# Kernel optimization log

Measured on AMD Instinct MI355X. Metric: run time of the kernel, lower is better.

Reference implementation:

```python
import jax, jax.numpy as jnp
import numpy as np

ALPHA = 0.25
GAMMA = 2.0
W_CLASS, W_BBOX, W_GIOU, W_EMBED = 1.0, 1.0, 1.0, 0.5
EPS = 1e-8


def box_cxcywh_to_xyxy(b):
    cx, cy, w, h = b[..., 0], b[..., 1], b[..., 2], b[..., 3]
    return jnp.stack([cx - 0.5 * w, cy - 0.5 * h, cx + 0.5 * w, cy + 0.5 * h], axis=-1)


def generalized_box_iou(boxes1, boxes2):
    # boxes1 [N,4], boxes2 [M,4] in xyxy -> [N,M]
    area1 = (boxes1[:, 2] - boxes1[:, 0]) * (boxes1[:, 3] - boxes1[:, 1])
    area2 = (boxes2[:, 2] - boxes2[:, 0]) * (boxes2[:, 3] - boxes2[:, 1])
    lt = jnp.maximum(boxes1[:, None, :2], boxes2[None, :, :2])  # [N,M,2]
    rb = jnp.minimum(boxes1[:, None, 2:], boxes2[None, :, 2:])
    wh = jnp.clip(rb - lt, 0.0)
    inter = wh[..., 0] * wh[..., 1]
    union = area1[:, None] + area2[None, :] - inter
    iou = inter / union
    lt_e = jnp.minimum(boxes1[:, None, :2], boxes2[None, :, :2])
    rb_e = jnp.maximum(boxes1[:, None, 2:], boxes2[None, :, 2:])
    wh_e = jnp.clip(rb_e - lt_e, 0.0)
    area_e = wh_e[..., 0] * wh_e[..., 1]
    return iou - (area_e - union) / area_e


def setup_inputs() -> dict:
    key = jax.random.key(0)
    ks = jax.random.split(key, 6)
    B, Q, C, D, M = 16, 1024, 91, 512, 1600
    pred_logits = jax.random.normal(ks[0], (B, Q, C), dtype=jnp.float32)
    pred_boxes = jax.random.uniform(ks[1], (B, Q, 4), dtype=jnp.float32)
    pred_embed = jax.random.normal(ks[2], (B, Q, D), dtype=jnp.float32)
    text_embeddings = jax.random.normal(ks[3], (C, D), dtype=jnp.float32)
    tgt_ids = jax.random.randint(ks[4], (M,), 0, C, dtype=jnp.int64 if jax.config.jax_enable_x64 else jnp.int32)
    tgt_bbox = jax.random.uniform(ks[5], (M, 4), dtype=jnp.float32)
    return {
        'pred_logits': pred_logits,
        'pred_boxes': pred_boxes,
        'pred_embed': pred_embed,
        'text_embeddings': text_embeddings,
        'tgt_ids': tgt_ids,
        'tgt_bbox': tgt_bbox,
    }


def reference(pred_logits, pred_boxes, pred_embed, text_embeddings, tgt_ids, tgt_bbox):
    B, Q, _ = pred_logits.shape
    N = B * Q
    # --- focal class cost on gathered target-class columns: [N, M]
    logits = pred_logits.reshape(N, -1)
    p = jax.nn.sigmoid(logits[:, tgt_ids])
    pos_cost = ALPHA * (1.0 - p) ** GAMMA * (-jnp.log(p + EPS))
    neg_cost = (1.0 - ALPHA) * p ** GAMMA * (-jnp.log(1.0 - p + EPS))
    cost_class = pos_cost - neg_cost
    # --- L1 box cost (cdist, p=1): [N, M]
    out_bbox = pred_boxes.reshape(N, 4)
    cost_bbox = jnp.sum(jnp.abs(out_bbox[:, None, :] - tgt_bbox[None, :, :]), axis=-1)
    # --- GIoU cost: [N, M]
    cost_giou = -generalized_box_iou(box_cxcywh_to_xyxy(out_bbox), box_cxcywh_to_xyxy(tgt_bbox))
    # --- embedding cosine cost: [N, M]
    v = pred_embed.reshape(N, -1)
    v = v / jnp.linalg.norm(v, axis=1, keepdims=True)
    te = text_embeddings[tgt_ids]  # [M, D]
    cost_embed = 1.0 - v @ te.T
    C = W_BBOX * cost_bbox + W_CLASS * cost_class + W_GIOU * cost_giou + W_EMBED * cost_embed
    return C.reshape(B, Q, -1)
```

## Files before the change

### kernel.cpp

```cpp
#include <hip/hip_runtime.h>
#include <hip/hip_bf16.h>

using bf16x8 = __attribute__((ext_vector_type(8))) short;
using f32x4  = __attribute__((ext_vector_type(4))) float;
using f32x2  = __attribute__((ext_vector_type(2))) float;

__device__ __forceinline__ unsigned short f2bf(float x) {
    unsigned int u = __float_as_uint(x);
    return (unsigned short)((u + 0x7FFFu + ((u >> 16) & 1u)) >> 16);
}

__global__ __launch_bounds__(256)
void k_prep(const float* __restrict__ te, unsigned short* __restrict__ te_bf) {
    const int r = blockIdx.x;
    for (int i = threadIdx.x; i < 512; i += 256) {
        const float v = (r < 91) ? te[(size_t)r * 512 + i] : 0.f;
        te_bf[(size_t)r * 512 + i] = f2bf(v);
    }
}

__global__ __launch_bounds__(256)
void k_class_embed(const float* __restrict__ logits,
                   const float* __restrict__ embed,
                   const unsigned short* __restrict__ te_bf,
                   float* __restrict__ ccombo)
{
    __shared__ float accs[4][16 * 96];
    __shared__ float sq_s[4][16];

    const int tid  = threadIdx.x;
    const int lane = tid & 63;
    const int wv   = tid >> 6;
    const int r16  = lane & 15;
    const int q    = lane >> 4;
    const int n0   = blockIdx.x * 16;

    f32x4 acc[6];
#pragma unroll
    for (int j = 0; j < 6; ++j) acc[j] = (f32x4){0.f, 0.f, 0.f, 0.f};
    float sumsq = 0.f;

    const float* arow = embed + (size_t)(n0 + r16) * 512 + wv * 128 + q * 8;
#pragma unroll
    for (int ks = 0; ks < 4; ++ks) {
        const float4 a0 = *(const float4*)(arow + ks * 32);
        const float4 a1 = *(const float4*)(arow + ks * 32 + 4);
        sumsq = __builtin_fmaf(a0.x, a0.x, sumsq);
        sumsq = __builtin_fmaf(a0.y, a0.y, sumsq);
        sumsq = __builtin_fmaf(a0.z, a0.z, sumsq);
        sumsq = __builtin_fmaf(a0.w, a0.w, sumsq);
        sumsq = __builtin_fmaf(a1.x, a1.x, sumsq);
        sumsq = __builtin_fmaf(a1.y, a1.y, sumsq);
        sumsq = __builtin_fmaf(a1.z, a1.z, sumsq);
        sumsq = __builtin_fmaf(a1.w, a1.w, sumsq);
        union { unsigned int u[4]; bf16x8 v; } cvt;
        asm("v_cvt_pk_bf16_f32 %0, %1, %2" : "=v"(cvt.u[0]) : "v"(a0.x), "v"(a0.y));
        asm("v_cvt_pk_bf16_f32 %0, %1, %2" : "=v"(cvt.u[1]) : "v"(a0.z), "v"(a0.w));
        asm("v_cvt_pk_bf16_f32 %0, %1, %2" : "=v"(cvt.u[2]) : "v"(a1.x), "v"(a1.y));
        asm("v_cvt_pk_bf16_f32 %0, %1, %2" : "=v"(cvt.u[3]) : "v"(a1.z), "v"(a1.w));
#pragma unroll
        for (int ct = 0; ct < 6; ++ct) {
            const bf16x8 bfr = *(const bf16x8*)(te_bf + (size_t)(ct * 16 + r16) * 512
                                                + wv * 128 + ks * 32 + q * 8);
            acc[ct] = __builtin_amdgcn_mfma_f32_16x16x32_bf16(cvt.v, bfr, acc[ct], 0, 0, 0);
        }
    }
    sumsq += __shfl_xor(sumsq, 16);
    sumsq += __shfl_xor(sumsq, 32);
    if (lane < 16) sq_s[wv][r16] = sumsq;

#pragma unroll
    for (int ct = 0; ct < 6; ++ct)
#pragma unroll
        for (int j = 0; j < 4; ++j)
            accs[wv][(q * 4 + j) * 96 + ct * 16 + r16] = acc[ct][j];
    __syncthreads();

#pragma unroll
    for (int i = 0; i < 6; ++i) {
        const int e = tid + i * 256;
        const int row = e / 96, col = e - row * 96;
        float v = 0.f;
        if (col < 91) {
            const float dot = accs[0][e] + accs[1][e] + accs[2][e] + accs[3][e];
            const float rn  = rsqrtf(sq_s[0][row] + sq_s[1][row] + sq_s[2][row] + sq_s[3][row]);
            const float x = logits[(size_t)(n0 + row) * 91 + col];
            const float p = 1.f / (1.f + __expf(-x));
            const float pos = 0.25f * (1.f - p) * (1.f - p) * (-__logf(p + 1e-8f));
            const float neg = 0.75f * p * p * (-__logf(1.f - p + 1e-8f));
            v = (pos - neg) + 0.5f - 0.5f * dot * rn;
        }
        ccombo[(size_t)n0 * 96 + e] = v;
    }
}

__device__ __forceinline__ float cost_core(
    float px0, float py0, float px1, float py1,
    float pcx, float pcy, float pw, float ph, float pa,
    float tx0, float ty0, float tx1, float ty1,
    float tcx, float tcy, float tw, float th, float ta, float cc)
{
    float res, t0, t1, t2, t3, t4, t5;
    asm("v_min_f32 %[t0], %[px1], %[tx1]\n\t"
        "v_max_f32 %[t1], %[px0], %[tx0]\n\t"
        "v_sub_f32 %[t0], %[t0], %[t1]\n\t"
        "v_min_f32 %[t1], %[py1], %[ty1]\n\t"
        "v_max_f32 %[t2], %[py0], %[ty0]\n\t"
        "v_sub_f32 %[t1], %[t1], %[t2]\n\t"
        "v_max_f32 %[t2], 0, %[t0]\n\t"
        "v_max_f32 %[t3], 0, %[t1]\n\t"
        "v_mul_f32 %[t4], %[t2], %[t3]\n\t"
        "v_add_f32 %[t2], %[pw], %[tw]\n\t"
        "v_sub_f32 %[t2], %[t2], %[t0]\n\t"
        "v_add_f32 %[t3], %[ph], %[th]\n\t"
        "v_sub_f32 %[t3], %[t3], %[t1]\n\t"
        "v_mul_f32 %[t0], %[t2], %[t3]\n\t"
        "v_add_f32 %[t1], %[pa], %[ta]\n\t"
        "v_sub_f32 %[t1], %[t1], %[t4]\n\t"
        "v_sub_f32 %[t2], %[t0], %[t1]\n\t"
        "v_mul_f32 %[t3], %[t1], %[t2]\n\t"
        "v_fma_f32 %[t2], %[t4], %[t0], -%[t3]\n\t"
        "v_mul_f32 %[t3], %[t1], %[t0]\n\t"
        "v_rcp_f32 %[t3], %[t3]\n\t"
        "v_sub_f32 %[t0], %[pcx], %[tcx]\n\t"
        "v_sub_f32 %[t1], %[pcy], %[tcy]\n\t"
        "v_add_f32 %[t4], |%[t0]|, |%[t1]|\n\t"
        "v_sub_f32 %[t0], %[pw], %[tw]\n\t"
        "v_sub_f32 %[t1], %[ph], %[th]\n\t"
        "v_add_f32 %[t5], |%[t0]|, |%[t1]|\n\t"
        "v_add_f32 %[t4], %[t4], %[t5]\n\t"
        "v_add_f32 %[t4], %[t4], %[cc]\n\t"
        "v_fma_f32 %[res], -%[t2], %[t3], %[t4]"
        : [res]"=v"(res), [t0]"=&v"(t0), [t1]"=&v"(t1), [t2]"=&v"(t2),
          [t3]"=&v"(t3), [t4]"=&v"(t4), [t5]"=&v"(t5)
        : [px0]"v"(px0), [py0]"v"(py0), [px1]"v"(px1), [py1]"v"(py1),
          [pcx]"v"(pcx), [pcy]"v"(pcy), [pw]"v"(pw), [ph]"v"(ph), [pa]"v"(pa),
          [tx0]"v"(tx0), [ty0]"v"(ty0), [tx1]"v"(tx1), [ty1]"v"(ty1),
          [tcx]"v"(tcx), [tcy]"v"(tcy), [tw]"v"(tw), [th]"v"(th), [ta]"v"(ta),
          [cc]"v"(cc));
    return res;
}

__global__ __launch_bounds__(256, 8)
void k_cost(const float* __restrict__ pboxes,
            const float* __restrict__ tboxes,
            const int*   __restrict__ tids,
            const float* __restrict__ ccombo,
            float* __restrict__ out)
{
    __shared__ float cc_s[32 * 96];
    __shared__ float p_s[32 * 12];

    const int tid = threadIdx.x;
    const int bx  = blockIdx.x;
    const int x      = bx & 7;
    const int i      = bx >> 3;
    const int nchunk = x + 8 * (i / 13);
    const int mchunk = i % 13;
    const int n0     = nchunk * 32;

    {
        const f32x4* src = (const f32x4*)(ccombo + (size_t)n0 * 96);
        f32x4* dst = (f32x4*)cc_s;
#pragma unroll
        for (int k = 0; k < 3; ++k) dst[tid + k * 256] = src[tid + k * 256];
    }
    if (tid < 32) {
        const float4 b = *(const float4*)(pboxes + (size_t)(n0 + tid) * 4);
        float* p = &p_s[tid * 12];
        p[0] = b.x; p[1] = b.y; p[2] = b.z; p[3] = b.w;
        p[4] = __builtin_fmaf(-0.5f, b.z, b.x);
        p[5] = __builtin_fmaf(-0.5f, b.w, b.y);
        p[6] = __builtin_fmaf( 0.5f, b.z, b.x);
        p[7] = __builtin_fmaf( 0.5f, b.w, b.y);
        p[8] = b.z * b.w;
    }

    const int lane = tid & 63;
    const int wv   = tid >> 6;
    const int m    = mchunk * 128 + lane * 2;
    const int mr   = (m < 1600) ? m : 1598;
    float tcx[2], tcy[2], tw[2], th[2];
    float tx0[2], ty0[2], tx1[2], ty1[2], ta[2];
#pragma unroll
    for (int j = 0; j < 2; ++j) {
        const float4 b = *(const float4*)(tboxes + (size_t)(mr + j) * 4);
        tcx[j] = b.x; tcy[j] = b.y; tw[j] = b.z; th[j] = b.w;
        tx0[j] = __builtin_fmaf(-0.5f, b.z, b.x);
        ty0[j] = __builtin_fmaf(-0.5f, b.w, b.y);
        tx1[j] = __builtin_fmaf( 0.5f, b.z, b.x);
        ty1[j] = __builtin_fmaf( 0.5f, b.w, b.y);
        ta[j]  = b.z * b.w;
    }
    const int2 idv = *(const int2*)(tids + mr);
    const int ids[2] = {idv.x, idv.y};
    __syncthreads();

    const int r8 = wv * 8;
    const bool do_store = (m < 1600);
    float* obase = out + (size_t)(n0 + r8) * 1600 + m;

#pragma unroll
    for (int p = 0; p < 8; ++p) {
        const float* pr = &p_s[(r8 + p) * 12];
        const float4 P0 = *(const float4*)pr;
        const float4 P1 = *(const float4*)(pr + 4);
        const float  pa = pr[8];
        const float* ccrow = &cc_s[(r8 + p) * 96];
        float res[2];
#pragma unroll
        for (int j = 0; j < 2; ++j) {
            res[j] = cost_core(P1.x, P1.y, P1.z, P1.w,
                               P0.x, P0.y, P0.z, P0.w, pa,
                               tx0[j], ty0[j], tx1[j], ty1[j],
                               tcx[j], tcy[j], tw[j], th[j], ta[j],
                               ccrow[ids[j]]);
        }
        if (do_store) {
            f32x2 r2 = {res[0], res[1]};
            *(f32x2*)(obase + (size_t)p * 1600) = r2;
        }
    }
}

extern "C" void kernel_launch(void* const* d_in, const int* in_sizes, int n_in,
                              void* d_out, int out_size, void* d_ws, size_t ws_size,
                              hipStream_t stream) {
    const float* pred_logits = (const float*)d_in[0];
    const float* pred_boxes  = (const float*)d_in[1];
    const float* pred_embed  = (const float*)d_in[2];
    const float* text_emb    = (const float*)d_in[3];
    const int*   tgt_ids     = (const int*)d_in[4];
    const float* tgt_bbox    = (const float*)d_in[5];
    float* out = (float*)d_out;

    unsigned short* te_bf = (unsigned short*)d_ws;
    float* ccombo = (float*)((char*)d_ws + 102400);

    k_prep<<<96, 256, 0, stream>>>(text_emb, te_bf);
    k_class_embed<<<1024, 256, 0, stream>>>(pred_logits, pred_embed, te_bf, ccombo);
    k_cost<<<512 * 13, 256, 0, stream>>>(pred_boxes, tgt_bbox, tgt_ids, ccombo, out);
}
```

Before: 53.89 us.

## Fuse class/embed cost and box cost into one kernel per 16-row block

Merges the MFMA class+embedding kernel and the box-cost kernel into one kernel. Each block computes the 16x96 combined class/embed table in shared memory and then writes the full 16x1600 output rows, staging all target boxes and ids in shared memory that reuses the GEMM scratch area. This drops the global ccombo round trip and one launch. In exchange the grid shrinks to 1024 blocks with a large shared footprint, each block re-stages all 1600 targets, and the store-bound phase has less parallelism.

New measurement: 50.72 us. -5.9%, faster.

```diff
diff --git a/kernel.cpp b/kernel.cpp
--- a/kernel.cpp
+++ b/kernel.cpp
@@ -16,81 +16,6 @@
     for (int i = threadIdx.x; i < 512; i += 256) {
         const float v = (r < 91) ? te[(size_t)r * 512 + i] : 0.f;
         te_bf[(size_t)r * 512 + i] = f2bf(v);
-    }
-}
-
-__global__ __launch_bounds__(256)
-void k_class_embed(const float* __restrict__ logits,
-                   const float* __restrict__ embed,
-                   const unsigned short* __restrict__ te_bf,
-                   float* __restrict__ ccombo)
-{
-    __shared__ float accs[4][16 * 96];
-    __shared__ float sq_s[4][16];
-
-    const int tid  = threadIdx.x;
-    const int lane = tid & 63;
-    const int wv   = tid >> 6;
-    const int r16  = lane & 15;
-    const int q    = lane >> 4;
-    const int n0   = blockIdx.x * 16;
-
-    f32x4 acc[6];
-#pragma unroll
-    for (int j = 0; j < 6; ++j) acc[j] = (f32x4){0.f, 0.f, 0.f, 0.f};
-    float sumsq = 0.f;
-
-    const float* arow = embed + (size_t)(n0 + r16) * 512 + wv * 128 + q * 8;
-#pragma unroll
-    for (int ks = 0; ks < 4; ++ks) {
-        const float4 a0 = *(const float4*)(arow + ks * 32);
-        const float4 a1 = *(const float4*)(arow + ks * 32 + 4);
-        sumsq = __builtin_fmaf(a0.x, a0.x, sumsq);
-        sumsq = __builtin_fmaf(a0.y, a0.y, sumsq);
-        sumsq = __builtin_fmaf(a0.z, a0.z, sumsq);
-        sumsq = __builtin_fmaf(a0.w, a0.w, sumsq);
-        sumsq = __builtin_fmaf(a1.x, a1.x, sumsq);
-        sumsq = __builtin_fmaf(a1.y, a1.y, sumsq);
-        sumsq = __builtin_fmaf(a1.z, a1.z, sumsq);
-        sumsq = __builtin_fmaf(a1.w, a1.w, sumsq);
-        union { unsigned int u[4]; bf16x8 v; } cvt;
-        asm("v_cvt_pk_bf16_f32 %0, %1, %2" : "=v"(cvt.u[0]) : "v"(a0.x), "v"(a0.y));
-        asm("v_cvt_pk_bf16_f32 %0, %1, %2" : "=v"(cvt.u[1]) : "v"(a0.z), "v"(a0.w));
-        asm("v_cvt_pk_bf16_f32 %0, %1, %2" : "=v"(cvt.u[2]) : "v"(a1.x), "v"(a1.y));
-        asm("v_cvt_pk_bf16_f32 %0, %1, %2" : "=v"(cvt.u[3]) : "v"(a1.z), "v"(a1.w));
-#pragma unroll
-        for (int ct = 0; ct < 6; ++ct) {
-            const bf16x8 bfr = *(const bf16x8*)(te_bf + (size_t)(ct * 16 + r16) * 512
-                                                + wv * 128 + ks * 32 + q * 8);
-            acc[ct] = __builtin_amdgcn_mfma_f32_16x16x32_bf16(cvt.v, bfr, acc[ct], 0, 0, 0);
-        }
-    }
-    sumsq += __shfl_xor(sumsq, 16);
-    sumsq += __shfl_xor(sumsq, 32);
-    if (lane < 16) sq_s[wv][r16] = sumsq;
-
-#pragma unroll
-    for (int ct = 0; ct < 6; ++ct)
-#pragma unroll
-        for (int j = 0; j < 4; ++j)
-            accs[wv][(q * 4 + j) * 96 + ct * 16 + r16] = acc[ct][j];
-    __syncthreads();
-
-#pragma unroll
-    for (int i = 0; i < 6; ++i) {
-        const int e = tid + i * 256;
-        const int row = e / 96, col = e - row * 96;
-        float v = 0.f;
-        if (col < 91) {
-            const float dot = accs[0][e] + accs[1][e] + accs[2][e] + accs[3][e];
-            const float rn  = rsqrtf(sq_s[0][row] + sq_s[1][row] + sq_s[2][row] + sq_s[3][row]);
-            const float x = logits[(size_t)(n0 + row) * 91 + col];
-            const float p = 1.f / (1.f + __expf(-x));
-            const float pos = 0.25f * (1.f - p) * (1.f - p) * (-__logf(p + 1e-8f));
-            const float neg = 0.75f * p * p * (-__logf(1.f - p + 1e-8f));
-            v = (pos - neg) + 0.5f - 0.5f * dot * rn;
-        }
-        ccombo[(size_t)n0 * 96 + e] = v;
     }
 }
 
@@ -141,31 +66,98 @@
     return res;
 }
 
-__global__ __launch_bounds__(256, 8)
-void k_cost(const float* __restrict__ pboxes,
-            const float* __restrict__ tboxes,
-            const int*   __restrict__ tids,
-            const float* __restrict__ ccombo,
-            float* __restrict__ out)
+__global__ __launch_bounds__(256, 4)
+void k_fused(const float* __restrict__ logits,
+             const float* __restrict__ pboxes,
+             const float* __restrict__ embed,
+             const unsigned short* __restrict__ te_bf,
+             const int* __restrict__ tids,
+             const float* __restrict__ tboxes,
+             float* __restrict__ out)
 {
-    __shared__ float cc_s[32 * 96];
-    __shared__ float p_s[32 * 12];
-
-    const int tid = threadIdx.x;
-    const int bx  = blockIdx.x;
-    const int x      = bx & 7;
-    const int i      = bx >> 3;
-    const int nchunk = x + 8 * (i / 13);
-    const int mchunk = i % 13;
-    const int n0     = nchunk * 32;
-
-    {
-        const f32x4* src = (const f32x4*)(ccombo + (size_t)n0 * 96);
-        f32x4* dst = (f32x4*)cc_s;
-#pragma unroll
-        for (int k = 0; k < 3; ++k) dst[tid + k * 256] = src[tid + k * 256];
-    }
-    if (tid < 32) {
+    union Region {
+        struct { float accs[4][1536]; float sq[4][16]; } g;
+        struct { float cx[1600], cy[1600], w[1600], h[1600];
+                 unsigned short id[1600]; } t;
+    };
+    __shared__ Region u;
+    __shared__ float cc_s[1536];
+    __shared__ float p_s[16 * 12];
+
+    const int tid  = threadIdx.x;
+    const int lane = tid & 63;
+    const int wv   = tid >> 6;
+    const int r16  = lane & 15;
+    const int q    = lane >> 4;
+    const int n0   = blockIdx.x * 16;
+
+    f32x4 acc[6];
+#pragma unroll
+    for (int j = 0; j < 6; ++j) acc[j] = (f32x4){0.f, 0.f, 0.f, 0.f};
+    float sumsq = 0.f;
+
+    const float* arow = embed + (size_t)(n0 + r16) * 512 + wv * 128 + q * 8;
+#pragma unroll
+    for (int ks = 0; ks < 4; ++ks) {
+        const float4 a0 = *(const float4*)(arow + ks * 32);
+        const float4 a1 = *(const float4*)(arow + ks * 32 + 4);
+        sumsq = __builtin_fmaf(a0.x, a0.x, sumsq);
+        sumsq = __builtin_fmaf(a0.y, a0.y, sumsq);
+        sumsq = __builtin_fmaf(a0.z, a0.z, sumsq);
+        sumsq = __builtin_fmaf(a0.w, a0.w, sumsq);
+        sumsq = __builtin_fmaf(a1.x, a1.x, sumsq);
+        sumsq = __builtin_fmaf(a1.y, a1.y, sumsq);
+        sumsq = __builtin_fmaf(a1.z, a1.z, sumsq);
+        sumsq = __builtin_fmaf(a1.w, a1.w, sumsq);
+        union { unsigned int uw[4]; bf16x8 v; } cvt;
+        asm("v_cvt_pk_bf16_f32 %0, %1, %2" : "=v"(cvt.uw[0]) : "v"(a0.x), "v"(a0.y));
+        asm("v_cvt_pk_bf16_f32 %0, %1, %2" : "=v"(cvt.uw[1]) : "v"(a0.z), "v"(a0.w));
+        asm("v_cvt_pk_bf16_f32 %0, %1, %2" : "=v"(cvt.uw[2]) : "v"(a1.x), "v"(a1.y));
+        asm("v_cvt_pk_bf16_f32 %0, %1, %2" : "=v"(cvt.uw[3]) : "v"(a1.z), "v"(a1.w));
+#pragma unroll
+        for (int ct = 0; ct < 6; ++ct) {
+            const bf16x8 bfr = *(const bf16x8*)(te_bf + (size_t)(ct * 16 + r16) * 512
+                                                + wv * 128 + ks * 32 + q * 8);
+            acc[ct] = __builtin_amdgcn_mfma_f32_16x16x32_bf16(cvt.v, bfr, acc[ct], 0, 0, 0);
+        }
+    }
+    sumsq += __shfl_xor(sumsq, 16);
+    sumsq += __shfl_xor(sumsq, 32);
+    if (lane < 16) u.g.sq[wv][r16] = sumsq;
+
+#pragma unroll
+    for (int ct = 0; ct < 6; ++ct)
+#pragma unroll
+        for (int j = 0; j < 4; ++j)
+            u.g.accs[wv][(q * 4 + j) * 96 + ct * 16 + r16] = acc[ct][j];
+    __syncthreads();
+
+#pragma unroll
+    for (int i = 0; i < 6; ++i) {
+        const int e = tid + i * 256;
+        const int row = e / 96, col = e - row * 96;
+        float v = 0.f;
+        if (col < 91) {
+            const float dot = u.g.accs[0][e] + u.g.accs[1][e]
+                            + u.g.accs[2][e] + u.g.accs[3][e];
+            const float rn = rsqrtf(u.g.sq[0][row] + u.g.sq[1][row]
+                                  + u.g.sq[2][row] + u.g.sq[3][row]);
+            const float x = logits[(size_t)(n0 + row) * 91 + col];
+            const float p = 1.f / (1.f + __expf(-x));
+            const float pos = 0.25f * (1.f - p) * (1.f - p) * (-__logf(p + 1e-8f));
+            const float neg = 0.75f * p * p * (-__logf(1.f - p + 1e-8f));
+            v = (pos - neg) + 0.5f - 0.5f * dot * rn;
+        }
+        cc_s[e] = v;
+    }
+    __syncthreads();
+
+    for (int m = tid; m < 1600; m += 256) {
+        const float4 b = *(const float4*)(tboxes + (size_t)m * 4);
+        u.t.cx[m] = b.x; u.t.cy[m] = b.y; u.t.w[m] = b.z; u.t.h[m] = b.w;
+        u.t.id[m] = (unsigned short)tids[m];
+    }
+    if (tid < 16) {
         const float4 b = *(const float4*)(pboxes + (size_t)(n0 + tid) * 4);
         float* p = &p_s[tid * 12];
         p[0] = b.x; p[1] = b.y; p[2] = b.z; p[3] = b.w;
@@ -175,50 +167,55 @@
         p[7] = __builtin_fmaf( 0.5f, b.w, b.y);
         p[8] = b.z * b.w;
     }
-
-    const int lane = tid & 63;
-    const int wv   = tid >> 6;
-    const int m    = mchunk * 128 + lane * 2;
-    const int mr   = (m < 1600) ? m : 1598;
-    float tcx[2], tcy[2], tw[2], th[2];
-    float tx0[2], ty0[2], tx1[2], ty1[2], ta[2];
-#pragma unroll
-    for (int j = 0; j < 2; ++j) {
-        const float4 b = *(const float4*)(tboxes + (size_t)(mr + j) * 4);
-        tcx[j] = b.x; tcy[j] = b.y; tw[j] = b.z; th[j] = b.w;
-        tx0[j] = __builtin_fmaf(-0.5f, b.z, b.x);
-        ty0[j] = __builtin_fmaf(-0.5f, b.w, b.y);
-        tx1[j] = __builtin_fmaf( 0.5f, b.z, b.x);
-        ty1[j] = __builtin_fmaf( 0.5f, b.w, b.y);
-        ta[j]  = b.z * b.w;
-    }
-    const int2 idv = *(const int2*)(tids + mr);
-    const int ids[2] = {idv.x, idv.y};
     __syncthreads();
 
-    const int r8 = wv * 8;
-    const bool do_store = (m < 1600);
-    float* obase = out + (size_t)(n0 + r8) * 1600 + m;
-
-#pragma unroll
-    for (int p = 0; p < 8; ++p) {
-        const float* pr = &p_s[(r8 + p) * 12];
-        const float4 P0 = *(const float4*)pr;
-        const float4 P1 = *(const float4*)(pr + 4);
-        const float  pa = pr[8];
-        const float* ccrow = &cc_s[(r8 + p) * 96];
-        float res[2];
+    const int r4 = wv * 4;
+#pragma unroll
+    for (int mc = 0; mc < 13; ++mc) {
+        const int m  = mc * 128 + lane * 2;
+        const bool valid = (m < 1600);
+        const int mr = valid ? m : 1598;
+
+        const f32x2 vcx = *(const f32x2*)&u.t.cx[mr];
+        const f32x2 vcy = *(const f32x2*)&u.t.cy[mr];
+        const f32x2 vw  = *(const f32x2*)&u.t.w[mr];
+        const f32x2 vh  = *(const f32x2*)&u.t.h[mr];
+        const unsigned int idp = *(const unsigned int*)&u.t.id[mr];
+        const int ids[2] = {(int)(idp & 0xffffu), (int)(idp >> 16)};
+
+        float tcx[2], tcy[2], tw[2], th[2];
+        float tx0[2], ty0[2], tx1[2], ty1[2], ta[2];
 #pragma unroll
         for (int j = 0; j < 2; ++j) {
-            res[j] = cost_core(P1.x, P1.y, P1.z, P1.w,
-                               P0.x, P0.y, P0.z, P0.w, pa,
-                               tx0[j], ty0[j], tx1[j], ty1[j],
-                               tcx[j], tcy[j], tw[j], th[j], ta[j],
-                               ccrow[ids[j]]);
-        }
-        if (do_store) {
-            f32x2 r2 = {res[0], res[1]};
-            *(f32x2*)(obase + (size_t)p * 1600) = r2;
+            tcx[j] = vcx[j]; tcy[j] = vcy[j]; tw[j] = vw[j]; th[j] = vh[j];
+            tx0[j] = __builtin_fmaf(-0.5f, tw[j], tcx[j]);
+            ty0[j] = __builtin_fmaf(-0.5f, th[j], tcy[j]);
+            tx1[j] = __builtin_fmaf( 0.5f, tw[j], tcx[j]);
+            ty1[j] = __builtin_fmaf( 0.5f, th[j], tcy[j]);
+            ta[j]  = tw[j] * th[j];
+        }
+
+#pragma unroll
+        for (int r = 0; r < 4; ++r) {
+            const int nl = r4 + r;
+            const float* pr = &p_s[nl * 12];
+            const float4 P0 = *(const float4*)pr;
+            const float4 P1 = *(const float4*)(pr + 4);
+            const float  pa = pr[8];
+            const float* ccrow = &cc_s[nl * 96];
+            float res[2];
+#pragma unroll
+            for (int j = 0; j < 2; ++j) {
+                res[j] = cost_core(P1.x, P1.y, P1.z, P1.w,
+                                   P0.x, P0.y, P0.z, P0.w, pa,
+                                   tx0[j], ty0[j], tx1[j], ty1[j],
+                                   tcx[j], tcy[j], tw[j], th[j], ta[j],
+                                   ccrow[ids[j]]);
+            }
+            if (valid) {
+                f32x2 r2 = {res[0], res[1]};
+                *(f32x2*)(out + (size_t)(n0 + nl) * 1600 + m) = r2;
+            }
         }
     }
 }
@@ -235,9 +232,8 @@
     float* out = (float*)d_out;
 
     unsigned short* te_bf = (unsigned short*)d_ws;
-    float* ccombo = (float*)((char*)d_ws + 102400);
 
     k_prep<<<96, 256, 0, stream>>>(text_emb, te_bf);
-    k_class_embed<<<1024, 256, 0, stream>>>(pred_logits, pred_embed, te_bf, ccombo);
-    k_cost<<<512 * 13, 256, 0, stream>>>(pred_boxes, tgt_bbox, tgt_ids, ccombo, out);
-}
+    k_fused<<<1024, 256, 0, stream>>>(pred_logits, pred_boxes, pred_embed,
+                                      te_bf, tgt_ids, tgt_bbox, out);
+}
```
